# Kernel optimization log

Measured on AMD Instinct MI355X. Metric: run time of the kernel, lower is better.

The kernel has to match this reference:

```python
import jax, jax.numpy as jnp
import numpy as np

B, N, EB, NA, DIM, NIT = 256, 128, 5, 64, 512, 3  # EB = n_bonds + 1 (channel 0 = no-bond, dropped)


def setup_inputs() -> dict:
    key = jax.random.key(0)
    ks = jax.random.split(key, 10)
    adj = jax.random.uniform(ks[0], (B, N, N, EB), dtype=jnp.float32)
    node = jax.random.normal(ks[1], (B, N, NA), dtype=jnp.float32)
    hidden = jnp.zeros((B, N, DIM), dtype=jnp.float32)  # accepted but unused by forward
    # nn.Linear default init: U(-1/sqrt(fan_in), 1/sqrt(fan_in))
    se = 1.0 / np.sqrt(NA)
    sd = 1.0 / np.sqrt(DIM)
    W_embed = jax.random.uniform(ks[2], (NA, DIM), minval=-se, maxval=se, dtype=jnp.float32)
    b_embed = jax.random.uniform(ks[3], (DIM,), minval=-se, maxval=se, dtype=jnp.float32)
    W_layers = jax.random.uniform(ks[4], (NIT, DIM, DIM), minval=-sd, maxval=sd, dtype=jnp.float32)
    b_layers = jax.random.uniform(ks[5], (NIT, DIM), minval=-sd, maxval=sd, dtype=jnp.float32)
    W_out = jax.random.uniform(ks[6], (DIM, 1), minval=-sd, maxval=sd, dtype=jnp.float32)
    b_out = jax.random.uniform(ks[7], (1,), minval=-sd, maxval=sd, dtype=jnp.float32)
    return {"adj": adj, "hidden": hidden, "node": node,
            "W_embed": W_embed, "b_embed": b_embed,
            "W_layers": W_layers, "b_layers": b_layers,
            "W_out": W_out, "b_out": b_out}


def reference(adj, hidden, node, W_embed, b_embed, W_layers, b_layers, W_out, b_out):
    # adj[:, :, :, 1:].permute(0, 3, 1, 2) -> [B, E, N, N]
    a = jnp.transpose(adj[..., 1:], (0, 3, 1, 2))
    h = node @ W_embed + b_embed  # [B, N, DIM]
    for i in range(NIT):  # WLSLinearLayer: relu(Linear(h + sum_e adj_e @ h))
        agg = jnp.einsum('benm,bmd->bnd', a, h)  # sum over bond types of neighbor aggregation
        h = jax.nn.relu((h + agg) @ W_layers[i] + b_layers[i])
    graph_repr = jnp.mean(h, axis=1)  # [B, DIM]
    logit = graph_repr @ W_out + b_out  # [B, 1], activation=None path
    return (logit, graph_repr)
```

## Files before the change

kernel.cpp:

```cpp
#include <hip/hip_runtime.h>
#include <hip/hip_bf16.h>


typedef __bf16 bf16;
typedef __bf16 bf16x4 __attribute__((ext_vector_type(4)));
typedef __bf16 bf16x8 __attribute__((ext_vector_type(8)));
typedef float floatx4 __attribute__((ext_vector_type(4)));

#define AS  136

__global__ __launch_bounds__(256) void k_pack(const float* __restrict__ We,
                                              const float* __restrict__ Wl,
                                              bf16* __restrict__ PWe,
                                              bf16* __restrict__ PWl) {
    __shared__ float S[512][17];
    int z = blockIdx.y, td = blockIdx.x;
    const float* src; bf16* dst; int K;
    if (z < 3) { src = Wl + (size_t)z * 262144; dst = PWl + (size_t)z * 262144; K = 512; }
    else       { src = We;                      dst = PWe;                      K = 64; }
    int tid = threadIdx.x;
    int x = tid & 15, y = tid >> 4;
    for (int kb = 0; kb < K; kb += 16) {
        int k = kb + y;
        S[k][x] = src[(size_t)k * 512 + td * 16 + x];
    }
    __syncthreads();
    int lane = tid & 63, w = tid >> 6, q = lane >> 4, l16 = lane & 15;
    int KT = K >> 5;
    for (int tk = w; tk < KT; tk += 4) {
        bf16x8 v;
#pragma unroll
        for (int j = 0; j < 8; j++) v[j] = (bf16)S[tk * 32 + q * 8 + j][l16];
        *(bf16x8*)&dst[(size_t)((td * KT + tk) * 64 + lane) * 8] = v;
    }
}

__global__ __launch_bounds__(1024, 4) void k_mega(
    const float* __restrict__ adj,
    const float* __restrict__ nodef,
    const bf16* __restrict__ PWe,
    const float* __restrict__ b_embed,
    const bf16* __restrict__ PWl,
    const float* __restrict__ b_layers,
    const float* __restrict__ W_out,
    const float* __restrict__ b_out,
    float* __restrict__ out)
{
    __shared__ __align__(16) char pool[135168];
    bf16* HT = (bf16*)pool;

    const int b = blockIdx.x;
    const int tid = threadIdx.x;
    const int lane = tid & 63, wid = tid >> 6;
    const int q = lane >> 4, l16 = lane & 15;

    bf16* AhatL = (bf16*)pool;
    {
        const float4* srcb = (const float4*)(adj + (size_t)b * 81920);
#pragma unroll 2
        for (int p = 0; p < 4; p++) {
            int t = p * 1024 + tid;
            const float4* ptr = srcb + (size_t)t * 5;
            float4 v0 = ptr[0], v1 = ptr[1], v2 = ptr[2], v3 = ptr[3], v4 = ptr[4];
            float s0 = v0.y + v0.z + v0.w + v1.x;
            float s1 = v1.z + v1.w + v2.x + v2.y;
            float s2 = v2.w + v3.x + v3.y + v3.z;
            float s3 = v4.x + v4.y + v4.z + v4.w;
            int n = t >> 5, m0 = (t & 31) * 4;
            bf16x4 o;
            o[0] = (bf16)(s0 + ((n == m0 + 0) ? 1.f : 0.f));
            o[1] = (bf16)(s1 + ((n == m0 + 1) ? 1.f : 0.f));
            o[2] = (bf16)(s2 + ((n == m0 + 2) ? 1.f : 0.f));
            o[3] = (bf16)(s3 + ((n == m0 + 3) ? 1.f : 0.f));
            *(bf16x4*)&AhatL[n * AS + m0] = o;
        }
    }
    __syncthreads();

    const int ntw = wid & 7, dh = wid >> 3;
    bf16x8 ahf[4];
#pragma unroll
    for (int kk = 0; kk < 4; kk++)
        ahf[kk] = *(const bf16x8*)&AhatL[(ntw * 16 + l16) * AS + kk * 32 + q * 8];
    __syncthreads();

    {
        const int wmE = wid >> 3, wnE = wid & 7;
        const float* Ab = nodef + (size_t)b * 8192;
        floatx4 accE[4][4] = {};
#pragma unroll
        for (int kk = 0; kk < 2; kk++) {
            bf16x8 af[4], bfr[4];
#pragma unroll
            for (int mt = 0; mt < 4; mt++) {
                const float* srcp = Ab + (size_t)(wmE * 64 + mt * 16 + l16) * 64 + kk * 32 + q * 8;
                float4 x = *(const float4*)srcp;
                float4 y = *(const float4*)(srcp + 4);
                bf16x8 v;
                v[0] = (bf16)x.x; v[1] = (bf16)x.y; v[2] = (bf16)x.z; v[3] = (bf16)x.w;
                v[4] = (bf16)y.x; v[5] = (bf16)y.y; v[6] = (bf16)y.z; v[7] = (bf16)y.w;
                af[mt] = v;
            }
#pragma unroll
            for (int nt = 0; nt < 4; nt++) {
                int td = wnE * 4 + nt;
                bfr[nt] = *(const bf16x8*)&PWe[(size_t)((td * 2 + kk) * 64 + lane) * 8];
            }
#pragma unroll
            for (int mt = 0; mt < 4; mt++)
#pragma unroll
                for (int nt = 0; nt < 4; nt++)
                    accE[mt][nt] = __builtin_amdgcn_mfma_f32_16x16x32_bf16(af[mt], bfr[nt], accE[mt][nt], 0, 0, 0);
        }
#pragma unroll
        for (int mt = 0; mt < 4; mt++)
#pragma unroll
            for (int nt = 0; nt < 4; nt++) {
                int d = wnE * 64 + nt * 16 + l16;
                float bv = b_embed[d];
                int c = wmE * 8 + mt * 2 + (q >> 1);
                int off = ((c ^ (d & 15)) << 3) + (q & 1) * 4;
                bf16x4 pk;
#pragma unroll
                for (int r = 0; r < 4; r++) pk[r] = (bf16)(accE[mt][nt][r] + bv);
                *(bf16x4*)&HT[d * 128 + off] = pk;
            }
    }
    __syncthreads();

    for (int it = 0; it < 3; it++) {
        const bf16* WT = PWl + (size_t)it * 262144;
        const float* bl = b_layers + it * 512;

        bf16x8 wf0 = *(const bf16x8*)&WT[(size_t)(((wid * 2 + 0) * 16 + 0) * 64 + lane) * 8];
        bf16x8 wf1 = *(const bf16x8*)&WT[(size_t)(((wid * 2 + 1) * 16 + 0) * 64 + lane) * 8];

        floatx4 at[16] = {};
#pragma unroll
        for (int dtile = 0; dtile < 16; dtile++) {
            int drow = dh * 256 + dtile * 16 + l16;
#pragma unroll
            for (int kk = 0; kk < 4; kk++) {
                int off = ((4 * kk + q) ^ (drow & 15)) << 3;
                bf16x8 af = *(const bf16x8*)&HT[drow * 128 + off];
                at[dtile] = __builtin_amdgcn_mfma_f32_16x16x32_bf16(af, ahf[kk], at[dtile], 0, 0, 0);
            }
        }
        __syncthreads();
        {
            int n = ntw * 16 + l16;
#pragma unroll
            for (int dtile = 0; dtile < 16; dtile++) {
                int c = dh * 32 + dtile * 2 + (q >> 1);
                int off = ((c ^ l16) << 3) + (q & 1) * 4;
                bf16x4 pk;
#pragma unroll
                for (int r = 0; r < 4; r++) pk[r] = (bf16)at[dtile][r];
                *(bf16x4*)&HT[n * 512 + off] = pk;
            }
        }
        __syncthreads();

        floatx4 acc[8][2] = {};
        for (int dc = 0; dc < 16; dc++) {
            int dcn = (dc + 1) & 15;
            bf16x8 nf0 = *(const bf16x8*)&WT[(size_t)(((wid * 2 + 0) * 16 + dcn) * 64 + lane) * 8];
            bf16x8 nf1 = *(const bf16x8*)&WT[(size_t)(((wid * 2 + 1) * 16 + dcn) * 64 + lane) * 8];
            int c = ((dc * 4 + q) ^ l16) << 3;
            bf16x8 afa[4];
#pragma unroll
            for (int mt = 0; mt < 4; mt++)
                afa[mt] = *(const bf16x8*)&HT[(mt * 16 + l16) * 512 + c];
#pragma unroll
            for (int mt = 0; mt < 4; mt++)
                acc[mt][0] = __builtin_amdgcn_mfma_f32_16x16x32_bf16(afa[mt], wf0, acc[mt][0], 0, 0, 0);
#pragma unroll
            for (int mt = 0; mt < 4; mt++)
                acc[mt][1] = __builtin_amdgcn_mfma_f32_16x16x32_bf16(afa[mt], wf1, acc[mt][1], 0, 0, 0);
            bf16x8 afb[4];
#pragma unroll
            for (int mt = 0; mt < 4; mt++)
                afb[mt] = *(const bf16x8*)&HT[((mt + 4) * 16 + l16) * 512 + c];
#pragma unroll
            for (int mt = 0; mt < 4; mt++)
                acc[mt + 4][0] = __builtin_amdgcn_mfma_f32_16x16x32_bf16(afb[mt], wf0, acc[mt + 4][0], 0, 0, 0);
#pragma unroll
            for (int mt = 0; mt < 4; mt++)
                acc[mt + 4][1] = __builtin_amdgcn_mfma_f32_16x16x32_bf16(afb[mt], wf1, acc[mt + 4][1], 0, 0, 0);
            wf0 = nf0; wf1 = nf1;
        }

        if (it < 2) {
            __syncthreads();
#pragma unroll
            for (int nt = 0; nt < 2; nt++) {
                int dp = wid * 32 + nt * 16 + l16;
                float bv = bl[dp];
#pragma unroll
                for (int mt = 0; mt < 8; mt++) {
                    int c = mt * 2 + (q >> 1);
                    int off = ((c ^ (dp & 15)) << 3) + (q & 1) * 4;
                    bf16x4 pk;
#pragma unroll
                    for (int r = 0; r < 4; r++) pk[r] = (bf16)fmaxf(acc[mt][nt][r] + bv, 0.f);
                    *(bf16x4*)&HT[dp * 128 + off] = pk;
                }
            }
            __syncthreads();
        } else {
            float* RsF = (float*)(pool + 131072);
#pragma unroll
            for (int nt = 0; nt < 2; nt++) {
                int dp = wid * 32 + nt * 16 + l16;
                float bv = bl[dp];
                float s = 0.f;
#pragma unroll
                for (int mt = 0; mt < 8; mt++)
#pragma unroll
                    for (int r = 0; r < 4; r++)
                        s += fmaxf(acc[mt][nt][r] + bv, 0.f);
                s += __shfl_down(s, 32);
                s += __shfl_down(s, 16);
                if (lane < 16) RsF[dp] = s;
            }
        }
    }
    __syncthreads();

    float* RsF = (float*)(pool + 131072);
    float* lpF = (float*)(pool + 131072 + 2048);
    if (tid < 512) {
        float g = RsF[tid] * (1.f / 128.f);
        out[256 + (size_t)b * 512 + tid] = g;
        lpF[tid] = g * W_out[tid];
    }
    __syncthreads();
    for (int s = 256; s > 0; s >>= 1) {
        if (tid < s) lpF[tid] += lpF[tid + s];
        __syncthreads();
    }
    if (tid == 0) out[b] = lpF[0] + b_out[0];
}

extern "C" void kernel_launch(void* const* d_in, const int* in_sizes, int n_in,
                              void* d_out, int out_size, void* d_ws, size_t ws_size,
                              hipStream_t stream) {
    const float* adj      = (const float*)d_in[0];
    const float* node     = (const float*)d_in[2];
    const float* W_embed  = (const float*)d_in[3];
    const float* b_embed  = (const float*)d_in[4];
    const float* W_layers = (const float*)d_in[5];
    const float* b_layers = (const float*)d_in[6];
    const float* W_out    = (const float*)d_in[7];
    const float* b_out    = (const float*)d_in[8];
    float* out = (float*)d_out;

    char* ws = (char*)d_ws;
    bf16* PWe = (bf16*)(ws);
    bf16* PWl = (bf16*)(ws + 65536);

    k_pack<<<dim3(32, 4), 256, 0, stream>>>(W_embed, W_layers, PWe, PWl);
    k_mega<<<256, 1024, 0, stream>>>(adj, node, PWe, b_embed, PWl, b_layers,
                                     W_out, b_out, out);
}
```

Baseline: 257.9 us.

## Retile neighbor aggregation into 4x4 MFMA register blocks with LDS-packed adjacency

```diff
diff --git a/kernel.cpp b/kernel.cpp
--- a/kernel.cpp
+++ b/kernel.cpp
@@ -46,8 +46,9 @@
     const float* __restrict__ b_out,
     float* __restrict__ out)
 {
-    __shared__ __align__(16) char pool[135168];
+    __shared__ __align__(16) char pool[163840];
     bf16* HT = (bf16*)pool;
+    bf16* AhatP = (bf16*)(pool + 131072);
 
     const int b = blockIdx.x;
     const int tid = threadIdx.x;
@@ -77,11 +78,15 @@
     }
     __syncthreads();
 
-    const int ntw = wid & 7, dh = wid >> 3;
-    bf16x8 ahf[4];
-#pragma unroll
-    for (int kk = 0; kk < 4; kk++)
-        ahf[kk] = *(const bf16x8*)&AhatL[(ntw * 16 + l16) * AS + kk * 32 + q * 8];
+    {
+        int j0 = wid * 2;
+#pragma unroll
+        for (int jj = 0; jj < 2; jj++) {
+            int j = j0 + jj, nt = j >> 2, kk = j & 3;
+            bf16x8 v = *(const bf16x8*)&AhatL[(nt * 16 + l16) * AS + kk * 32 + q * 8];
+            *(bf16x8*)&AhatP[(size_t)((nt * 4 + kk) * 64 + lane) * 8] = v;
+        }
+    }
     __syncthreads();
 
     {
@@ -128,44 +133,62 @@
     }
     __syncthreads();
 
+    const int nh = wid & 1, dg = wid >> 1;
+
     for (int it = 0; it < 3; it++) {
         const bf16* WT = PWl + (size_t)it * 262144;
         const float* bl = b_layers + it * 512;
 
-        bf16x8 wf0 = *(const bf16x8*)&WT[(size_t)(((wid * 2 + 0) * 16 + 0) * 64 + lane) * 8];
-        bf16x8 wf1 = *(const bf16x8*)&WT[(size_t)(((wid * 2 + 1) * 16 + 0) * 64 + lane) * 8];
-
-        floatx4 at[16] = {};
-#pragma unroll
-        for (int dtile = 0; dtile < 16; dtile++) {
-            int drow = dh * 256 + dtile * 16 + l16;
-#pragma unroll
-            for (int kk = 0; kk < 4; kk++) {
+        const bf16* Wb0 = WT + (size_t)(wid * 2 + 0) * 8192 + lane * 8;
+        const bf16* Wb1 = WT + (size_t)(wid * 2 + 1) * 8192 + lane * 8;
+
+        bf16x8 w00 = *(const bf16x8*)Wb0;
+        bf16x8 w01 = *(const bf16x8*)Wb1;
+
+        floatx4 at[4][4] = {};
+#pragma unroll
+        for (int kk = 0; kk < 4; kk++) {
+            bf16x8 bfr[4];
+#pragma unroll
+            for (int nt = 0; nt < 4; nt++)
+                bfr[nt] = *(const bf16x8*)&AhatP[(size_t)(((nh * 4 + nt) * 4 + kk) * 64 + lane) * 8];
+            bf16x8 afr[4];
+#pragma unroll
+            for (int dt = 0; dt < 4; dt++) {
+                int drow = dg * 64 + dt * 16 + l16;
                 int off = ((4 * kk + q) ^ (drow & 15)) << 3;
-                bf16x8 af = *(const bf16x8*)&HT[drow * 128 + off];
-                at[dtile] = __builtin_amdgcn_mfma_f32_16x16x32_bf16(af, ahf[kk], at[dtile], 0, 0, 0);
-            }
+                afr[dt] = *(const bf16x8*)&HT[drow * 128 + off];
+            }
+#pragma unroll
+            for (int dt = 0; dt < 4; dt++)
+#pragma unroll
+                for (int nt = 0; nt < 4; nt++)
+                    at[dt][nt] = __builtin_amdgcn_mfma_f32_16x16x32_bf16(afr[dt], bfr[nt], at[dt][nt], 0, 0, 0);
         }
         __syncthreads();
         {
-            int n = ntw * 16 + l16;
-#pragma unroll
-            for (int dtile = 0; dtile < 16; dtile++) {
-                int c = dh * 32 + dtile * 2 + (q >> 1);
-                int off = ((c ^ l16) << 3) + (q & 1) * 4;
-                bf16x4 pk;
-#pragma unroll
-                for (int r = 0; r < 4; r++) pk[r] = (bf16)at[dtile][r];
-                *(bf16x4*)&HT[n * 512 + off] = pk;
-            }
+#pragma unroll
+            for (int dt = 0; dt < 4; dt++)
+#pragma unroll
+                for (int nt = 0; nt < 4; nt++) {
+                    int n = nh * 64 + nt * 16 + l16;
+                    int c = dg * 8 + dt * 2 + (q >> 1);
+                    int off = ((c ^ l16) << 3) + (q & 1) * 4;
+                    bf16x4 pk;
+#pragma unroll
+                    for (int r = 0; r < 4; r++) pk[r] = (bf16)at[dt][nt][r];
+                    *(bf16x4*)&HT[n * 512 + off] = pk;
+                }
         }
         __syncthreads();
 
         floatx4 acc[8][2] = {};
+        bf16x8 w10 = *(const bf16x8*)(Wb0 + 512);
+        bf16x8 w11 = *(const bf16x8*)(Wb1 + 512);
         for (int dc = 0; dc < 16; dc++) {
-            int dcn = (dc + 1) & 15;
-            bf16x8 nf0 = *(const bf16x8*)&WT[(size_t)(((wid * 2 + 0) * 16 + dcn) * 64 + lane) * 8];
-            bf16x8 nf1 = *(const bf16x8*)&WT[(size_t)(((wid * 2 + 1) * 16 + dcn) * 64 + lane) * 8];
+            int dcn = (dc + 2) & 15;
+            bf16x8 n0 = *(const bf16x8*)(Wb0 + dcn * 512);
+            bf16x8 n1 = *(const bf16x8*)(Wb1 + dcn * 512);
             int c = ((dc * 4 + q) ^ l16) << 3;
             bf16x8 afa[4];
 #pragma unroll
@@ -173,21 +196,21 @@
                 afa[mt] = *(const bf16x8*)&HT[(mt * 16 + l16) * 512 + c];
 #pragma unroll
             for (int mt = 0; mt < 4; mt++)
-                acc[mt][0] = __builtin_amdgcn_mfma_f32_16x16x32_bf16(afa[mt], wf0, acc[mt][0], 0, 0, 0);
-#pragma unroll
-            for (int mt = 0; mt < 4; mt++)
-                acc[mt][1] = __builtin_amdgcn_mfma_f32_16x16x32_bf16(afa[mt], wf1, acc[mt][1], 0, 0, 0);
+                acc[mt][0] = __builtin_amdgcn_mfma_f32_16x16x32_bf16(afa[mt], w00, acc[mt][0], 0, 0, 0);
+#pragma unroll
+            for (int mt = 0; mt < 4; mt++)
+                acc[mt][1] = __builtin_amdgcn_mfma_f32_16x16x32_bf16(afa[mt], w01, acc[mt][1], 0, 0, 0);
             bf16x8 afb[4];
 #pragma unroll
             for (int mt = 0; mt < 4; mt++)
                 afb[mt] = *(const bf16x8*)&HT[((mt + 4) * 16 + l16) * 512 + c];
 #pragma unroll
             for (int mt = 0; mt < 4; mt++)
-                acc[mt + 4][0] = __builtin_amdgcn_mfma_f32_16x16x32_bf16(afb[mt], wf0, acc[mt + 4][0], 0, 0, 0);
-#pragma unroll
-            for (int mt = 0; mt < 4; mt++)
-                acc[mt + 4][1] = __builtin_amdgcn_mfma_f32_16x16x32_bf16(afb[mt], wf1, acc[mt + 4][1], 0, 0, 0);
-            wf0 = nf0; wf1 = nf1;
+                acc[mt + 4][0] = __builtin_amdgcn_mfma_f32_16x16x32_bf16(afb[mt], w00, acc[mt + 4][0], 0, 0, 0);
+#pragma unroll
+            for (int mt = 0; mt < 4; mt++)
+                acc[mt + 4][1] = __builtin_amdgcn_mfma_f32_16x16x32_bf16(afb[mt], w01, acc[mt + 4][1], 0, 0, 0);
+            w00 = w10; w01 = w11; w10 = n0; w11 = n1;
         }
 
         if (it < 2) {
@@ -235,11 +258,18 @@
         lpF[tid] = g * W_out[tid];
     }
     __syncthreads();
-    for (int s = 256; s > 0; s >>= 1) {
-        if (tid < s) lpF[tid] += lpF[tid + s];
-        __syncthreads();
-    }
-    if (tid == 0) out[b] = lpF[0] + b_out[0];
+    if (wid == 0) {
+        float s = 0.f;
+#pragma unroll
+        for (int k = 0; k < 8; k++) s += lpF[lane + k * 64];
+        s += __shfl_down(s, 32);
+        s += __shfl_down(s, 16);
+        s += __shfl_down(s, 8);
+        s += __shfl_down(s, 4);
+        s += __shfl_down(s, 2);
+        s += __shfl_down(s, 1);
+        if (lane == 0) out[b] = s + b_out[0];
+    }
 }
 
 extern "C" void kernel_launch(void* const* d_in, const int* in_sizes, int n_in,
```

After: 242.7 us. 5.9% less time.
